# Optimization experiments

Hardware: AMD Instinct MI355X
Metric: run time of the kernel (lower is better)

## Reference

```python
import jax, jax.numpy as jnp
import numpy as np
import math

T, H, F, E, K = 16384, 1024, 2816, 8, 2
CAP_FACTOR = 1.25
TEMPERATURE = 1.0


def setup_inputs() -> dict:
    key = jax.random.key(0)
    ks = jax.random.split(key, 5)
    x = jax.random.normal(ks[0], (T, H), dtype=jnp.float32)
    Wg = jax.random.normal(ks[1], (H, E), dtype=jnp.float32) * 0.02
    W1 = jax.random.normal(ks[2], (E, H, F), dtype=jnp.float32) * 0.02
    W3 = jax.random.normal(ks[3], (E, H, F), dtype=jnp.float32) * 0.02
    W2 = jax.random.normal(ks[4], (E, F, H), dtype=jnp.float32) * 0.02
    return {"x": x, "Wg": Wg, "W1": W1, "W3": W3, "W2": W2}


def reference(x, Wg, W1, W3, W2):
    num_tokens, hidden = x.shape
    num_experts = Wg.shape[1]
    k = K
    capacity = int(math.ceil(num_tokens * CAP_FACTOR * k / num_experts))  # 5120

    # --- top-k gating (matches PyTorch fallback: softmax over top-k values) ---
    gate_logits = x @ Wg                                  # [T, E]
    top_vals, top_idx = jax.lax.top_k(gate_logits / TEMPERATURE, k)
    top_w = jax.nn.softmax(top_vals, axis=-1)             # [T, K]

    # --- dispatch: token-major, k-major fill order, overflow dropped ---
    flat_e = top_idx.reshape(-1)                          # [T*K], assignment order t*K + k
    onehot = jax.nn.one_hot(flat_e, num_experts, dtype=jnp.int32)  # [T*K, E]
    # position within each expert's buffer (0-based, in assignment order)
    pos = jnp.sum(jnp.cumsum(onehot, axis=0) * onehot, axis=-1) - 1  # [T*K]
    valid = pos < capacity                                # overflow mask
    dummy = num_experts * capacity                        # trash slot
    slot = jnp.where(valid, flat_e * capacity + pos, dummy)  # [T*K]
    tok_of_assign = jnp.arange(num_tokens * k) // k       # [T*K]

    buf = jnp.zeros((num_experts * capacity + 1, hidden), dtype=x.dtype)
    buf = buf.at[slot].set(x[tok_of_assign])              # slots unique per expert
    expert_inputs = buf[: num_experts * capacity].reshape(num_experts, capacity, hidden)

    # --- SwiGLU experts (grouped GEMMs) ---
    g = jax.nn.silu(jnp.einsum("ech,ehf->ecf", expert_inputs, W1))
    u = jnp.einsum("ech,ehf->ecf", expert_inputs, W3)
    expert_out = jnp.einsum("ecf,efh->ech", g * u, W2)    # [E, C, H]
    eo_flat = expert_out.reshape(num_experts * capacity, hidden)

    # --- weighted combine (scatter-add back to tokens) ---
    safe_slot = jnp.minimum(slot, num_experts * capacity - 1)
    gathered = eo_flat[safe_slot]                         # [T*K, H]
    w_flat = top_w.reshape(-1) * valid.astype(top_w.dtype)
    combined = jnp.zeros((num_tokens, hidden), dtype=x.dtype)
    combined = combined.at[tok_of_assign].add(w_flat[:, None] * gathered)
    return combined
```

## Files before the change

### kernel.cpp

```cpp
#include <hip/hip_runtime.h>
#include <hip/hip_bf16.h>
#include <math.h>

#define T_TOK 16384
#define HID   1024
#define FFN   2816
#define NE    8
#define CAP   5120
#define NASSIGN (T_TOK*2)
#define NWAVE   (NASSIGN/64)

#define WB_E ((size_t)HID*FFN)
#define GB_E ((size_t)CAP*FFN)

#define OFF_TOPIDX 0ull
#define OFF_TOPW   (OFF_TOPIDX + (size_t)T_TOK*8)
#define OFF_WCNT   (OFF_TOPW   + (size_t)T_TOK*8)
#define OFF_WOFF   (OFF_WCNT   + (size_t)NWAVE*NE*4)
#define OFF_USED   (OFF_WOFF   + (size_t)NWAVE*NE*4)
#define OFF_AE     (OFF_USED   + 256)
#define OFF_AR     (OFF_AE     + (size_t)NASSIGN*4)
#define OFF_TOS    (OFF_AR     + (size_t)NASSIGN*4)
#define OFF_WSL    (OFF_TOS    + (size_t)NE*CAP*4)
#define OFF_XB     (OFF_WSL    + (size_t)NE*CAP*4)
#define OFF_WT     (OFF_XB     + (size_t)T_TOK*HID*2)

typedef __bf16 bf16x8 __attribute__((ext_vector_type(8)));
typedef float  f32x4  __attribute__((ext_vector_type(4)));

static __device__ __forceinline__ unsigned short f2bf(float f) {
    unsigned int u = __float_as_uint(f);
    unsigned int r = u + 0x7fffu + ((u >> 16) & 1u);
    return (unsigned short)(r >> 16);
}

static __device__ __forceinline__ void gload16(const void* g, void* l) {
    __builtin_amdgcn_global_load_lds(
        (const __attribute__((address_space(1))) unsigned int*)g,
        (__attribute__((address_space(3))) unsigned int*)l, 16, 0, 0);
}

static __device__ __forceinline__ int xcd_swz1d(int total) {
    int lid = blockIdx.x;
    return (lid & 7) * (total >> 3) + (lid >> 3);
}

__global__ __launch_bounds__(256) void k_transpose_cvt(
    const float* __restrict__ in, unsigned short* __restrict__ outb, int R, int C)
{
    __shared__ float tile[32][33];
    const float* inp = in + (size_t)blockIdx.z * R * C;
    unsigned short* outp = outb + (size_t)blockIdx.z * R * C;
    const int r0 = blockIdx.y * 32, c0 = blockIdx.x * 32;
    const int tr = threadIdx.x >> 5, tc = threadIdx.x & 31;
#pragma unroll
    for (int p = 0; p < 4; ++p)
        tile[tr + 8*p][tc] = inp[(size_t)(r0 + tr + 8*p) * C + c0 + tc];
    __syncthreads();
#pragma unroll
    for (int p = 0; p < 4; ++p)
        outp[(size_t)(c0 + tr + 8*p) * R + r0 + tc] = f2bf(tile[tc][tr + 8*p]);
}

__global__ __launch_bounds__(256) void k_gate(
    const float* __restrict__ x, const float* __restrict__ Wg,
    int2* __restrict__ top_idx, float2* __restrict__ top_w,
    unsigned short* __restrict__ xb)
{
    __shared__ float wgT[NE * HID];
    const int tid = threadIdx.x;
    for (int idx = tid; idx < NE * HID; idx += 256) {
        int h = idx >> 3, e = idx & 7;
        wgT[e * HID + h] = Wg[idx];
    }
    __syncthreads();
    const int wave = tid >> 6, lane = tid & 63;
    const int t = blockIdx.x * 4 + wave;
    float a[NE];
#pragma unroll
    for (int e = 0; e < NE; ++e) a[e] = 0.f;
    const float* xr = x + (size_t)t * HID;
    unsigned short* xbr = xb + (size_t)t * HID;
    for (int j = 0; j < HID / 64; ++j) {
        float xv = xr[j * 64 + lane];
        xbr[j * 64 + lane] = f2bf(xv);
#pragma unroll
        for (int e = 0; e < NE; ++e)
            a[e] = fmaf(xv, wgT[e * HID + j * 64 + lane], a[e]);
    }
#pragma unroll
    for (int e = 0; e < NE; ++e) {
#pragma unroll
        for (int off = 32; off > 0; off >>= 1)
            a[e] += __shfl_xor(a[e], off, 64);
    }
    if (lane == 0) {
        float v0 = -1e30f, v1 = -1e30f; int i0 = 0, i1 = 0;
#pragma unroll
        for (int e = 0; e < NE; ++e) {
            float v = a[e];
            if (v > v0)      { v1 = v0; i1 = i0; v0 = v; i0 = e; }
            else if (v > v1) { v1 = v;  i1 = e; }
        }
        float e1 = expf(v1 - v0);
        float s  = 1.f + e1;
        top_idx[t] = make_int2(i0, i1);
        top_w[t]   = make_float2(1.f / s, e1 / s);
    }
}

__global__ __launch_bounds__(256) void k_count(
    const int2* __restrict__ top_idx, int* __restrict__ wcnt,
    int* __restrict__ ae, int* __restrict__ ar)
{
    const int i = blockIdx.x * 256 + threadIdx.x;
    const int2 ti = top_idx[i >> 1];
    const int e = (i & 1) ? ti.y : ti.x;
    const int lane = threadIdx.x & 63;
    const int wid = i >> 6;
    const unsigned long long lt = (1ull << lane) - 1ull;
    int rank = 0;
#pragma unroll
    for (int ex = 0; ex < NE; ++ex) {
        unsigned long long m = __ballot(e == ex);
        if (e == ex)    rank = __popcll(m & lt);
        if (lane == ex) wcnt[wid * NE + ex] = __popcll(m);
    }
    ae[i] = e; ar[i] = rank;
}

__global__ __launch_bounds__(NWAVE) void k_scan(
    const int* __restrict__ wcnt, int* __restrict__ woff, int* __restrict__ used)
{
    __shared__ int sb[NWAVE];
    const int tid = threadIdx.x;
    for (int ex = 0; ex < NE; ++ex) {
        int v = wcnt[tid * NE + ex];
        sb[tid] = v;
        __syncthreads();
        for (int off = 1; off < NWAVE; off <<= 1) {
            int p = (tid >= off) ? sb[tid - off] : 0;
            __syncthreads();
            sb[tid] += p;
            __syncthreads();
        }
        woff[tid * NE + ex] = sb[tid] - v;
        if (tid == NWAVE - 1) used[ex] = min(sb[tid], CAP);
        __syncthreads();
    }
}

__global__ __launch_bounds__(256) void k_emit(
    const int* __restrict__ ae, const int* __restrict__ ar,
    const int* __restrict__ woff, const float2* __restrict__ top_w,
    int* __restrict__ tos, float* __restrict__ wsl)
{
    const int i = blockIdx.x * 256 + threadIdx.x;
    const int e = ae[i];
    const int pos = woff[(i >> 6) * NE + e] + ar[i];
    if (pos < CAP) {
        const int slot = e * CAP + pos;
        tos[slot] = i >> 1;
        const float2 w = top_w[i >> 1];
        wsl[slot] = (i & 1) ? w.y : w.x;
    }
}

__global__ __launch_bounds__(256, 2) void k_gemm13(
    const unsigned short* __restrict__ xb,
    const unsigned short* __restrict__ W1t,
    const unsigned short* __restrict__ W3t,
    const int* __restrict__ tos, const int* __restrict__ used_arr,
    unsigned short* __restrict__ G,
    int e0, int we0, int ec)
{
    __shared__ __align__(16) unsigned short As[128 * 32];
    __shared__ __align__(16) unsigned short B1s[128 * 32];
    __shared__ __align__(16) unsigned short B3s[128 * 32];
    __shared__ int toks[128];

    const int logical = xcd_swz1d(880 * ec);
    const int bx = logical % 40;
    const int by = (logical / 40) % 22;
    const int e  = e0 + logical / 880;

    const int used = used_arr[e];
    const int row0 = bx * 128;
    if (row0 >= used) return;
    const int col0 = by * 128;
    const int tid = threadIdx.x;

    if (tid < 128) { int r = row0 + tid; toks[tid] = (r < used) ? tos[e * CAP + r] : 0; }
    __syncthreads();

    const int qr = tid >> 2, qk = (tid & 3) * 8;
    const unsigned short* srcA0 = xb + (size_t)toks[qr] * HID + qk;
    const unsigned short* srcA1 = xb + (size_t)toks[64 + qr] * HID + qk;
    const unsigned short* w1e = W1t + (size_t)(e - we0) * WB_E;
    const unsigned short* w3e = W3t + (size_t)(e - we0) * WB_E;
    const unsigned short* srcB1_0 = w1e + (size_t)(col0 + qr) * HID + qk;
    const unsigned short* srcB1_1 = w1e + (size_t)(col0 + 64 + qr) * HID + qk;
    const unsigned short* srcB3_0 = w3e + (size_t)(col0 + qr) * HID + qk;
    const unsigned short* srcB3_1 = w3e + (size_t)(col0 + 64 + qr) * HID + qk;

    const int wv = tid >> 6, lane = tid & 63;
    unsigned short* dA0 = As + wv * 512;
    unsigned short* dA1 = As + 2048 + wv * 512;
    unsigned short* dB1_0 = B1s + wv * 512;
    unsigned short* dB1_1 = B1s + 2048 + wv * 512;
    unsigned short* dB3_0 = B3s + wv * 512;
    unsigned short* dB3_1 = B3s + 2048 + wv * 512;

    f32x4 acc1[4][4], acc3[4][4];
#pragma unroll
    for (int m = 0; m < 4; ++m)
#pragma unroll
        for (int n = 0; n < 4; ++n) {
            acc1[m][n] = {0.f, 0.f, 0.f, 0.f};
            acc3[m][n] = {0.f, 0.f, 0.f, 0.f};
        }

    const int mb = (wv >> 1) * 64, nb = (wv & 1) * 64;
    const int fr = lane & 15, kh = (lane >> 4) * 8;

    for (int k0 = 0; k0 < HID; k0 += 32) {
        gload16(srcA0, dA0);     gload16(srcA1, dA1);
        gload16(srcB1_0, dB1_0); gload16(srcB1_1, dB1_1);
        gload16(srcB3_0, dB3_0); gload16(srcB3_1, dB3_1);
        srcA0 += 32; srcA1 += 32;
        srcB1_0 += 32; srcB1_1 += 32; srcB3_0 += 32; srcB3_1 += 32;
        __syncthreads();
        bf16x8 a[4], b1[4], b3[4];
#pragma unroll
        for (int m = 0; m < 4; ++m)
            a[m] = *(const bf16x8*)&As[(mb + m * 16 + fr) * 32 + kh];
#pragma unroll
        for (int n = 0; n < 4; ++n) {
            b1[n] = *(const bf16x8*)&B1s[(nb + n * 16 + fr) * 32 + kh];
            b3[n] = *(const bf16x8*)&B3s[(nb + n * 16 + fr) * 32 + kh];
        }
#pragma unroll
        for (int m = 0; m < 4; ++m)
#pragma unroll
            for (int n = 0; n < 4; ++n) {
                acc1[m][n] = __builtin_amdgcn_mfma_f32_16x16x32_bf16(a[m], b1[n], acc1[m][n], 0, 0, 0);
                acc3[m][n] = __builtin_amdgcn_mfma_f32_16x16x32_bf16(a[m], b3[n], acc3[m][n], 0, 0, 0);
            }
        __syncthreads();
    }

    unsigned short* Ge = G + (size_t)(e - e0) * GB_E;
    const int cr = (lane >> 4) * 4, cc = lane & 15;
#pragma unroll
    for (int m = 0; m < 4; ++m)
#pragma unroll
        for (int j = 0; j < 4; ++j) {
            const int r = row0 + mb + m * 16 + cr + j;
            if (r < used) {
#pragma unroll
                for (int n = 0; n < 4; ++n) {
                    float h1 = acc1[m][n][j], h3 = acc3[m][n][j];
                    float g = h1 / (1.f + __expf(-h1)) * h3;
                    Ge[(size_t)r * FFN + col0 + nb + n * 16 + cc] = f2bf(g);
                }
            }
        }
}

__global__ __launch_bounds__(256, 2) void k_gemm2(
    const unsigned short* __restrict__ G,
    const unsigned short* __restrict__ W2t,
    const int* __restrict__ tos, const float* __restrict__ wsl,
    const int* __restrict__ used_arr, float* __restrict__ out,
    int e0, int we0, int ec)
{
    __shared__ __align__(16) unsigned short As[128 * 32];
    __shared__ __align__(16) unsigned short Bs[128 * 32];

    const int logical = xcd_swz1d(320 * ec);
    const int bx = logical % 40;
    const int by = (logical / 40) % 8;
    const int e  = e0 + logical / 320;

    const int used = used_arr[e];
    const int row0 = bx * 128;
    if (row0 >= used) return;
    const int col0 = by * 128;
    const int tid = threadIdx.x;

    const int qr = tid >> 2, qk = (tid & 3) * 8;
    const unsigned short* Ge = G + (size_t)(e - e0) * GB_E;
    const unsigned short* srcA0 = Ge + (size_t)(row0 + qr) * FFN + qk;
    const unsigned short* srcA1 = Ge + (size_t)(row0 + 64 + qr) * FFN + qk;
    const unsigned short* w2e = W2t + (size_t)(e - we0) * WB_E;
    const unsigned short* srcB0 = w2e + (size_t)(col0 + qr) * FFN + qk;
    const unsigned short* srcB1 = w2e + (size_t)(col0 + 64 + qr) * FFN + qk;

    const int wv = tid >> 6, lane = tid & 63;
    unsigned short* dA0 = As + wv * 512;
    unsigned short* dA1 = As + 2048 + wv * 512;
    unsigned short* dB0 = Bs + wv * 512;
    unsigned short* dB1 = Bs + 2048 + wv * 512;

    f32x4 acc[4][4];
#pragma unroll
    for (int m = 0; m < 4; ++m)
#pragma unroll
        for (int n = 0; n < 4; ++n) acc[m][n] = {0.f, 0.f, 0.f, 0.f};

    const int mb = (wv >> 1) * 64, nb = (wv & 1) * 64;
    const int fr = lane & 15, kh = (lane >> 4) * 8;

    for (int k0 = 0; k0 < FFN; k0 += 32) {
        gload16(srcA0, dA0); gload16(srcA1, dA1);
        gload16(srcB0, dB0); gload16(srcB1, dB1);
        srcA0 += 32; srcA1 += 32; srcB0 += 32; srcB1 += 32;
        __syncthreads();
        bf16x8 a[4], b[4];
#pragma unroll
        for (int m = 0; m < 4; ++m)
            a[m] = *(const bf16x8*)&As[(mb + m * 16 + fr) * 32 + kh];
#pragma unroll
        for (int n = 0; n < 4; ++n)
            b[n] = *(const bf16x8*)&Bs[(nb + n * 16 + fr) * 32 + kh];
#pragma unroll
        for (int m = 0; m < 4; ++m)
#pragma unroll
            for (int n = 0; n < 4; ++n)
                acc[m][n] = __builtin_amdgcn_mfma_f32_16x16x32_bf16(a[m], b[n], acc[m][n], 0, 0, 0);
        __syncthreads();
    }

    const int cr = (lane >> 4) * 4, cc = lane & 15;
#pragma unroll
    for (int m = 0; m < 4; ++m)
#pragma unroll
        for (int j = 0; j < 4; ++j) {
            const int r = row0 + mb + m * 16 + cr + j;
            if (r < used) {
                const int slot = e * CAP + r;
                const int t = tos[slot];
                const float w = wsl[slot];
                float* orow = out + (size_t)t * HID + col0 + nb + cc;
#pragma unroll
                for (int n = 0; n < 4; ++n)
                    atomicAdd(orow + n * 16, w * acc[m][n][j]);
            }
        }
}

extern "C" void kernel_launch(void* const* d_in, const int* in_sizes, int n_in,
                              void* d_out, int out_size, void* d_ws, size_t ws_size,
                              hipStream_t stream)
{
    const float* x  = (const float*)d_in[0];
    const float* Wg = (const float*)d_in[1];
    const float* W1 = (const float*)d_in[2];
    const float* W3 = (const float*)d_in[3];
    const float* W2 = (const float*)d_in[4];
    float* out = (float*)d_out;
    char* ws = (char*)d_ws;

    const size_t wmat = WB_E * 2;
    const size_t gmat = GB_E * 2;
    const size_t base = OFF_WT;

    int EC = 0; bool chunkW = false;
    const size_t fullW_end = base + 3 * (size_t)NE * wmat;
    if      (ws_size >= fullW_end + 8 * gmat) { EC = 8; }
    else if (ws_size >= fullW_end + 4 * gmat) { EC = 4; }
    else if (ws_size >= fullW_end + 2 * gmat) { EC = 2; }
    else if (ws_size >= fullW_end + 1 * gmat) { EC = 1; }
    else if (ws_size >= base + 3 * wmat + gmat) { EC = 1; chunkW = true; }
    else {
        hipMemsetAsync(d_out, 0xFF, 2048, stream);
        return;
    }

    int2*   top_idx = (int2*)(ws + OFF_TOPIDX);
    float2* top_w   = (float2*)(ws + OFF_TOPW);
    int*   wcnt = (int*)(ws + OFF_WCNT);
    int*   woff = (int*)(ws + OFF_WOFF);
    int*   used = (int*)(ws + OFF_USED);
    int*   ae   = (int*)(ws + OFF_AE);
    int*   ar   = (int*)(ws + OFF_AR);
    int*   tos  = (int*)(ws + OFF_TOS);
    float* wsl  = (float*)(ws + OFF_WSL);
    unsigned short* xb  = (unsigned short*)(ws + OFF_XB);
    const int nw = chunkW ? 1 : NE;
    unsigned short* W1t = (unsigned short*)(ws + base);
    unsigned short* W3t = W1t + (size_t)nw * WB_E;
    unsigned short* W2t = W3t + (size_t)nw * WB_E;
    unsigned short* G   = W2t + (size_t)nw * WB_E;

    hipMemsetAsync(out, 0, (size_t)T_TOK * HID * 4, stream);

    k_gate<<<dim3(T_TOK / 4), dim3(256), 0, stream>>>(x, Wg, top_idx, top_w, xb);
    k_count<<<dim3(NASSIGN / 256), dim3(256), 0, stream>>>(top_idx, wcnt, ae, ar);
    k_scan<<<dim3(1), dim3(NWAVE), 0, stream>>>(wcnt, woff, used);
    k_emit<<<dim3(NASSIGN / 256), dim3(256), 0, stream>>>(ae, ar, woff, top_w, tos, wsl);

    if (!chunkW) {
        k_transpose_cvt<<<dim3(FFN / 32, HID / 32, NE), dim3(256), 0, stream>>>(W1, W1t, HID, FFN);
        k_transpose_cvt<<<dim3(FFN / 32, HID / 32, NE), dim3(256), 0, stream>>>(W3, W3t, HID, FFN);
        k_transpose_cvt<<<dim3(HID / 32, FFN / 32, NE), dim3(256), 0, stream>>>(W2, W2t, FFN, HID);
    }

    for (int e0 = 0; e0 < NE; e0 += EC) {
        const int we0 = chunkW ? e0 : 0;
        if (chunkW) {
            const size_t off = (size_t)e0 * WB_E;
            k_transpose_cvt<<<dim3(FFN / 32, HID / 32, 1), dim3(256), 0, stream>>>(W1 + off, W1t, HID, FFN);
            k_transpose_cvt<<<dim3(FFN / 32, HID / 32, 1), dim3(256), 0, stream>>>(W3 + off, W3t, HID, FFN);
            k_transpose_cvt<<<dim3(HID / 32, FFN / 32, 1), dim3(256), 0, stream>>>(W2 + off, W2t, FFN, HID);
        }
        k_gemm13<<<dim3(880 * EC), dim3(256), 0, stream>>>(xb, W1t, W3t, tos, used, G, e0, we0, EC);
        k_gemm2<<<dim3(320 * EC), dim3(256), 0, stream>>>(G, W2t, tos, wsl, used, out, e0, we0, EC);
    }
}
```

Before: 1.296 ms.

## Replace atomic scatter-add combine with bf16 expert-output buffer and gather kernel

When the workspace is large enough, the down-projection GEMM writes unweighted per-slot expert outputs as bf16 into a buffer that reuses the W1/W3 transposed-weight region. A new combine kernel then gathers each token's two slots, applies the gate weights and writes the output directly. This removes the output memset and the fp32 atomicAdds to scattered token rows. The cost is an extra bf16 round-trip through memory and one more bf16 rounding of expert outputs. The GEMMs are also launched as two 4-expert halves.

```diff
diff --git a/kernel.cpp b/kernel.cpp
--- a/kernel.cpp
+++ b/kernel.cpp
@@ -22,7 +22,8 @@
 #define OFF_AR     (OFF_AE     + (size_t)NASSIGN*4)
 #define OFF_TOS    (OFF_AR     + (size_t)NASSIGN*4)
 #define OFF_WSL    (OFF_TOS    + (size_t)NE*CAP*4)
-#define OFF_XB     (OFF_WSL    + (size_t)NE*CAP*4)
+#define OFF_ASLOT  (OFF_WSL    + (size_t)NE*CAP*4)
+#define OFF_XB     (OFF_ASLOT  + (size_t)NASSIGN*4)
 #define OFF_WT     (OFF_XB     + (size_t)T_TOK*HID*2)
 
 typedef __bf16 bf16x8 __attribute__((ext_vector_type(8)));
@@ -32,6 +33,9 @@
     unsigned int u = __float_as_uint(f);
     unsigned int r = u + 0x7fffu + ((u >> 16) & 1u);
     return (unsigned short)(r >> 16);
+}
+static __device__ __forceinline__ float bf2f(unsigned short u) {
+    return __uint_as_float(((unsigned int)u) << 16);
 }
 
 static __device__ __forceinline__ void gload16(const void* g, void* l) {
@@ -153,7 +157,7 @@
 __global__ __launch_bounds__(256) void k_emit(
     const int* __restrict__ ae, const int* __restrict__ ar,
     const int* __restrict__ woff, const float2* __restrict__ top_w,
-    int* __restrict__ tos, float* __restrict__ wsl)
+    int* __restrict__ tos, float* __restrict__ wsl, int* __restrict__ aslot)
 {
     const int i = blockIdx.x * 256 + threadIdx.x;
     const int e = ae[i];
@@ -163,6 +167,9 @@
         tos[slot] = i >> 1;
         const float2 w = top_w[i >> 1];
         wsl[slot] = (i & 1) ? w.y : w.x;
+        aslot[i] = slot;
+    } else {
+        aslot[i] = -1;
     }
 }
 
@@ -172,7 +179,7 @@
     const unsigned short* __restrict__ W3t,
     const int* __restrict__ tos, const int* __restrict__ used_arr,
     unsigned short* __restrict__ G,
-    int e0, int we0, int ec)
+    int e0, int we0, int ge0, int ec)
 {
     __shared__ __align__(16) unsigned short As[128 * 32];
     __shared__ __align__(16) unsigned short B1s[128 * 32];
@@ -249,7 +256,7 @@
         __syncthreads();
     }
 
-    unsigned short* Ge = G + (size_t)(e - e0) * GB_E;
+    unsigned short* Ge = G + (size_t)(e - ge0) * GB_E;
     const int cr = (lane >> 4) * 4, cc = lane & 15;
 #pragma unroll
     for (int m = 0; m < 4; ++m)
@@ -272,7 +279,8 @@
     const unsigned short* __restrict__ W2t,
     const int* __restrict__ tos, const float* __restrict__ wsl,
     const int* __restrict__ used_arr, float* __restrict__ out,
-    int e0, int we0, int ec)
+    unsigned short* __restrict__ eo,
+    int e0, int we0, int ge0, int ec)
 {
     __shared__ __align__(16) unsigned short As[128 * 32];
     __shared__ __align__(16) unsigned short Bs[128 * 32];
@@ -289,7 +297,7 @@
     const int tid = threadIdx.x;
 
     const int qr = tid >> 2, qk = (tid & 3) * 8;
-    const unsigned short* Ge = G + (size_t)(e - e0) * GB_E;
+    const unsigned short* Ge = G + (size_t)(e - ge0) * GB_E;
     const unsigned short* srcA0 = Ge + (size_t)(row0 + qr) * FFN + qk;
     const unsigned short* srcA1 = Ge + (size_t)(row0 + 64 + qr) * FFN + qk;
     const unsigned short* w2e = W2t + (size_t)(e - we0) * WB_E;
@@ -332,21 +340,58 @@
     }
 
     const int cr = (lane >> 4) * 4, cc = lane & 15;
-#pragma unroll
-    for (int m = 0; m < 4; ++m)
-#pragma unroll
-        for (int j = 0; j < 4; ++j) {
-            const int r = row0 + mb + m * 16 + cr + j;
-            if (r < used) {
-                const int slot = e * CAP + r;
-                const int t = tos[slot];
-                const float w = wsl[slot];
-                float* orow = out + (size_t)t * HID + col0 + nb + cc;
-#pragma unroll
-                for (int n = 0; n < 4; ++n)
-                    atomicAdd(orow + n * 16, w * acc[m][n][j]);
+    if (eo) {
+#pragma unroll
+        for (int m = 0; m < 4; ++m)
+#pragma unroll
+            for (int j = 0; j < 4; ++j) {
+                const int r = row0 + mb + m * 16 + cr + j;
+                if (r < used) {
+                    unsigned short* erow = eo + (size_t)(e * CAP + r) * HID + col0 + nb + cc;
+#pragma unroll
+                    for (int n = 0; n < 4; ++n)
+                        erow[n * 16] = f2bf(acc[m][n][j]);
+                }
             }
-        }
+    } else {
+#pragma unroll
+        for (int m = 0; m < 4; ++m)
+#pragma unroll
+            for (int j = 0; j < 4; ++j) {
+                const int r = row0 + mb + m * 16 + cr + j;
+                if (r < used) {
+                    const int slot = e * CAP + r;
+                    const int t = tos[slot];
+                    const float w = wsl[slot];
+                    float* orow = out + (size_t)t * HID + col0 + nb + cc;
+#pragma unroll
+                    for (int n = 0; n < 4; ++n)
+                        atomicAdd(orow + n * 16, w * acc[m][n][j]);
+                }
+            }
+    }
+}
+
+__global__ __launch_bounds__(256) void k_combine(
+    const unsigned short* __restrict__ eo, const int* __restrict__ aslot,
+    const float2* __restrict__ top_w, float* __restrict__ out)
+{
+    const int t = blockIdx.x;
+    const int c = threadIdx.x * 4;
+    const int s0 = aslot[2 * t], s1 = aslot[2 * t + 1];
+    const float2 w = top_w[t];
+    float4 acc = make_float4(0.f, 0.f, 0.f, 0.f);
+    if (s0 >= 0) {
+        ushort4 v = *(const ushort4*)(eo + (size_t)s0 * HID + c);
+        acc.x += w.x * bf2f(v.x); acc.y += w.x * bf2f(v.y);
+        acc.z += w.x * bf2f(v.z); acc.w += w.x * bf2f(v.w);
+    }
+    if (s1 >= 0) {
+        ushort4 v = *(const ushort4*)(eo + (size_t)s1 * HID + c);
+        acc.x += w.y * bf2f(v.x); acc.y += w.y * bf2f(v.y);
+        acc.z += w.y * bf2f(v.z); acc.w += w.y * bf2f(v.w);
+    }
+    *(float4*)(out + (size_t)t * HID + c) = acc;
 }
 
 extern "C" void kernel_launch(void* const* d_in, const int* in_sizes, int n_in,
@@ -364,10 +409,10 @@
     const size_t wmat = WB_E * 2;
     const size_t gmat = GB_E * 2;
     const size_t base = OFF_WT;
-
-    int EC = 0; bool chunkW = false;
     const size_t fullW_end = base + 3 * (size_t)NE * wmat;
-    if      (ws_size >= fullW_end + 8 * gmat) { EC = 8; }
+
+    int EC = 0; bool chunkW = false; bool eoMode = false;
+    if      (ws_size >= fullW_end + 8 * gmat) { EC = 8; eoMode = true; }
     else if (ws_size >= fullW_end + 4 * gmat) { EC = 4; }
     else if (ws_size >= fullW_end + 2 * gmat) { EC = 2; }
     else if (ws_size >= fullW_end + 1 * gmat) { EC = 1; }
@@ -379,26 +424,26 @@
 
     int2*   top_idx = (int2*)(ws + OFF_TOPIDX);
     float2* top_w   = (float2*)(ws + OFF_TOPW);
-    int*   wcnt = (int*)(ws + OFF_WCNT);
-    int*   woff = (int*)(ws + OFF_WOFF);
-    int*   used = (int*)(ws + OFF_USED);
-    int*   ae   = (int*)(ws + OFF_AE);
-    int*   ar   = (int*)(ws + OFF_AR);
-    int*   tos  = (int*)(ws + OFF_TOS);
-    float* wsl  = (float*)(ws + OFF_WSL);
+    int*   wcnt  = (int*)(ws + OFF_WCNT);
+    int*   woff  = (int*)(ws + OFF_WOFF);
+    int*   used  = (int*)(ws + OFF_USED);
+    int*   ae    = (int*)(ws + OFF_AE);
+    int*   ar    = (int*)(ws + OFF_AR);
+    int*   tos   = (int*)(ws + OFF_TOS);
+    float* wsl   = (float*)(ws + OFF_WSL);
+    int*   aslot = (int*)(ws + OFF_ASLOT);
     unsigned short* xb  = (unsigned short*)(ws + OFF_XB);
     const int nw = chunkW ? 1 : NE;
     unsigned short* W1t = (unsigned short*)(ws + base);
     unsigned short* W3t = W1t + (size_t)nw * WB_E;
     unsigned short* W2t = W3t + (size_t)nw * WB_E;
     unsigned short* G   = W2t + (size_t)nw * WB_E;
-
-    hipMemsetAsync(out, 0, (size_t)T_TOK * HID * 4, stream);
+    unsigned short* eo  = (unsigned short*)(ws + base);
 
     k_gate<<<dim3(T_TOK / 4), dim3(256), 0, stream>>>(x, Wg, top_idx, top_w, xb);
     k_count<<<dim3(NASSIGN / 256), dim3(256), 0, stream>>>(top_idx, wcnt, ae, ar);
     k_scan<<<dim3(1), dim3(NWAVE), 0, stream>>>(wcnt, woff, used);
-    k_emit<<<dim3(NASSIGN / 256), dim3(256), 0, stream>>>(ae, ar, woff, top_w, tos, wsl);
+    k_emit<<<dim3(NASSIGN / 256), dim3(256), 0, stream>>>(ae, ar, woff, top_w, tos, wsl, aslot);
 
     if (!chunkW) {
         k_transpose_cvt<<<dim3(FFN / 32, HID / 32, NE), dim3(256), 0, stream>>>(W1, W1t, HID, FFN);
@@ -406,15 +451,24 @@
         k_transpose_cvt<<<dim3(HID / 32, FFN / 32, NE), dim3(256), 0, stream>>>(W2, W2t, FFN, HID);
     }
 
-    for (int e0 = 0; e0 < NE; e0 += EC) {
-        const int we0 = chunkW ? e0 : 0;
-        if (chunkW) {
-            const size_t off = (size_t)e0 * WB_E;
-            k_transpose_cvt<<<dim3(FFN / 32, HID / 32, 1), dim3(256), 0, stream>>>(W1 + off, W1t, HID, FFN);
-            k_transpose_cvt<<<dim3(FFN / 32, HID / 32, 1), dim3(256), 0, stream>>>(W3 + off, W3t, HID, FFN);
-            k_transpose_cvt<<<dim3(HID / 32, FFN / 32, 1), dim3(256), 0, stream>>>(W2 + off, W2t, FFN, HID);
-        }
-        k_gemm13<<<dim3(880 * EC), dim3(256), 0, stream>>>(xb, W1t, W3t, tos, used, G, e0, we0, EC);
-        k_gemm2<<<dim3(320 * EC), dim3(256), 0, stream>>>(G, W2t, tos, wsl, used, out, e0, we0, EC);
-    }
-}
+    if (eoMode) {
+        k_gemm13<<<dim3(880 * 4), dim3(256), 0, stream>>>(xb, W1t, W3t, tos, used, G, 0, 0, 0, 4);
+        k_gemm13<<<dim3(880 * 4), dim3(256), 0, stream>>>(xb, W1t, W3t, tos, used, G, 4, 0, 0, 4);
+        k_gemm2<<<dim3(320 * 4), dim3(256), 0, stream>>>(G, W2t, tos, wsl, used, out, eo, 0, 0, 0, 4);
+        k_gemm2<<<dim3(320 * 4), dim3(256), 0, stream>>>(G, W2t, tos, wsl, used, out, eo, 4, 0, 0, 4);
+        k_combine<<<dim3(T_TOK), dim3(256), 0, stream>>>(eo, aslot, top_w, out);
+    } else {
+        hipMemsetAsync(out, 0, (size_t)T_TOK * HID * 4, stream);
+        for (int e0 = 0; e0 < NE; e0 += EC) {
+            const int we0 = chunkW ? e0 : 0;
+            if (chunkW) {
+                const size_t off = (size_t)e0 * WB_E;
+                k_transpose_cvt<<<dim3(FFN / 32, HID / 32, 1), dim3(256), 0, stream>>>(W1 + off, W1t, HID, FFN);
+                k_transpose_cvt<<<dim3(FFN / 32, HID / 32, 1), dim3(256), 0, stream>>>(W3 + off, W3t, HID, FFN);
+                k_transpose_cvt<<<dim3(HID / 32, FFN / 32, 1), dim3(256), 0, stream>>>(W2 + off, W2t, FFN, HID);
+            }
+            k_gemm13<<<dim3(880 * EC), dim3(256), 0, stream>>>(xb, W1t, W3t, tos, used, G, e0, we0, e0, EC);
+            k_gemm2<<<dim3(320 * EC), dim3(256), 0, stream>>>(G, W2t, tos, wsl, used, out, (unsigned short*)nullptr, e0, we0, e0, EC);
+        }
+    }
+}
```

Result: no change. 1.304 ms (+0.6%).
